# Kernel tuning notes

Measured on AMD Instinct MI355X. Metric: run time of the kernel, lower is better.

Reference implementation:

```python
import jax, jax.numpy as jnp
import numpy as np

B, S, E, H = 4, 8192, 768, 12
Dh = E // H


def setup_inputs() -> dict:
    key = jax.random.key(0)
    ks = jax.random.split(key, 11)
    scale = 1.0 / np.sqrt(E)
    return {
        "query": jax.random.normal(ks[0], (B, S, E), dtype=jnp.float32),
        "key": jax.random.normal(ks[1], (B, S, E), dtype=jnp.float32),
        "value": jax.random.normal(ks[2], (B, S, E), dtype=jnp.float32),
        "Wq": jax.random.normal(ks[3], (E, E), dtype=jnp.float32) * scale,
        "bq": jax.random.normal(ks[4], (E,), dtype=jnp.float32) * scale,
        "Wk": jax.random.normal(ks[5], (E, E), dtype=jnp.float32) * scale,
        "bk": jax.random.normal(ks[6], (E,), dtype=jnp.float32) * scale,
        "Wv": jax.random.normal(ks[7], (E, E), dtype=jnp.float32) * scale,
        "bv": jax.random.normal(ks[8], (E,), dtype=jnp.float32) * scale,
        "Wo": jax.random.normal(ks[9], (E, E), dtype=jnp.float32) * scale,
        "bo": jax.random.normal(ks[10], (E,), dtype=jnp.float32) * scale,
    }


def reference(query, key, value, Wq, bq, Wk, bk, Wv, bv, Wo, bo):
    b, s, e = query.shape
    # torch nn.Linear: x @ W.T + b
    Q = query @ Wq.T + bq  # [B,S,E]
    K = key @ Wk.T + bk
    V = value @ Wv.T + bv
    Q = Q.reshape(b, s, H, Dh)
    K = K.reshape(b, s, H, Dh)
    V = V.reshape(b, s, H, Dh)
    # ReLU feature map on Q and K
    Q = jax.nn.relu(Q)
    K = jax.nn.relu(K)
    # KV aggregation: [B,H,Dh,Dh]
    KV = jnp.einsum('blhd,blhe->bhde', K, V)
    # Query contraction: [B,S,H,Dh]
    QKV = jnp.einsum('blhd,bhde->blhe', Q, KV)
    QKV = QKV.reshape(b, s, e)
    return QKV @ Wo.T + bo
```

## Files before the change

### kernel.cpp

```cpp
#include <hip/hip_runtime.h>
#include <hip/hip_bf16.h>
#include <string.h>


#define H_  12
#define DH  64
#define E_  768
#define S_  8192
#define B_  4

typedef unsigned short u16;
typedef __attribute__((ext_vector_type(4))) float f32x4;
typedef __attribute__((ext_vector_type(4))) u16   u16x4;
typedef __attribute__((ext_vector_type(8))) u16   u16x8;
typedef __attribute__((ext_vector_type(8))) short s16x8;

static __device__ __forceinline__ u16 f2bf(float f) {
    __hip_bfloat16 h = __float2bfloat16(f);
    u16 r; __builtin_memcpy(&r, &h, 2); return r;
}
static __device__ __forceinline__ float bf2f(u16 u) {
    unsigned int i = ((unsigned int)u) << 16;
    float f; __builtin_memcpy(&f, &i, 4); return f;
}

static __device__ __forceinline__ void gload16(const void* g, void* lds) {
    __builtin_amdgcn_global_load_lds(
        (const __attribute__((address_space(1))) unsigned int*)(uintptr_t)g,
        (__attribute__((address_space(3))) unsigned int*)(uintptr_t)lds,
        16, 0, 0);
}

__global__ __launch_bounds__(256) void wconv(const float* __restrict__ in,
                                             u16* __restrict__ out, int n) {
    int i = (blockIdx.x * 256 + threadIdx.x) * 4;
    if (i + 3 < n) {
        f32x4 v = *(const f32x4*)&in[i];
        u16x4 o;
        o[0] = f2bf(v[0]); o[1] = f2bf(v[1]); o[2] = f2bf(v[2]); o[3] = f2bf(v[3]);
        *(u16x4*)&out[i] = o;
    }
}

__global__ __launch_bounds__(256) void xconv(const float* __restrict__ in,
                                             u16* __restrict__ out) {
    long i = ((long)blockIdx.x * 256 + threadIdx.x) * 8;
    f32x4 a = *(const f32x4*)&in[i];
    f32x4 b = *(const f32x4*)&in[i + 4];
    u16x8 o;
    o[0] = f2bf(a[0]); o[1] = f2bf(a[1]); o[2] = f2bf(a[2]); o[3] = f2bf(a[3]);
    o[4] = f2bf(b[0]); o[5] = f2bf(b[1]); o[6] = f2bf(b[2]); o[7] = f2bf(b[3]);
    *(u16x8*)&out[i] = o;
}

template<int RELU, int OUT_F32, int PERB>
__global__ __launch_bounds__(256, 2) void gemm4(const u16* __restrict__ A,
                                                const u16* __restrict__ Bw0,
                                                const float* __restrict__ bias,
                                                void* __restrict__ Cp, int K) {
    __shared__ u16 As[3][4096];
    __shared__ u16 Bs[3][8192];
    const int  t    = threadIdx.x;
    const int  lane = t & 63;
    const int  wave = t >> 6;
    const long m0   = (long)blockIdx.y * 128;
    const long n0   = (long)blockIdx.x * 256;
    const int  wr   = (wave >> 1) * 64;
    const int  wc   = (wave & 1) * 128;
    const int  N    = gridDim.x * 256;
    const u16* Bw   = PERB ? (Bw0 + (long)(blockIdx.y >> 6) * 589824L) : Bw0;

    const u16* srcA[2]; int dstA[2];
    #pragma unroll
    for (int c = 0; c < 2; ++c) {
        int ch   = wave * 2 + c;
        int o    = ch * 1024 + lane * 16;
        int lrow = o >> 7;
        int bir  = (o & 127) ^ ((lrow & 7) << 4);
        int row  = 2 * lrow + (bir >> 6);
        dstA[c]  = ch * 1024;
        srcA[c]  = A + (m0 + row) * (long)K + ((bir & 63) >> 1);
    }
    const u16* srcB[4]; int dstB[4];
    #pragma unroll
    for (int c = 0; c < 4; ++c) {
        int ch   = wave * 4 + c;
        int o    = ch * 1024 + lane * 16;
        int lrow = o >> 7;
        int bir  = (o & 127) ^ ((lrow & 7) << 4);
        int row  = 2 * lrow + (bir >> 6);
        dstB[c]  = ch * 1024;
        srcB[c]  = Bw + (n0 + row) * (long)K + ((bir & 63) >> 1);
    }

    const int kg16 = (lane >> 4) * 16;
    int aoff[4], boff[8];
    #pragma unroll
    for (int mi = 0; mi < 4; ++mi) {
        int m    = wr + mi * 16 + (lane & 15);
        int lrow = m >> 1;
        aoff[mi] = lrow * 128 + ((((m & 1) << 6) | kg16) ^ ((lrow & 7) << 4));
    }
    #pragma unroll
    for (int ni = 0; ni < 8; ++ni) {
        int n    = wc + ni * 16 + (lane & 15);
        int lrow = n >> 1;
        boff[ni] = lrow * 128 + ((((n & 1) << 6) | kg16) ^ ((lrow & 7) << 4));
    }

    f32x4 acc[4][8] = {};

    const int nt = K >> 5;
    #pragma unroll
    for (int c = 0; c < 2; ++c) gload16(srcA[c],      (char*)&As[0][0] + dstA[c]);
    #pragma unroll
    for (int c = 0; c < 4; ++c) gload16(srcB[c],      (char*)&Bs[0][0] + dstB[c]);
    #pragma unroll
    for (int c = 0; c < 2; ++c) gload16(srcA[c] + 32, (char*)&As[1][0] + dstA[c]);
    #pragma unroll
    for (int c = 0; c < 4; ++c) gload16(srcB[c] + 32, (char*)&Bs[1][0] + dstB[c]);

    int sl = 0;
    for (int tt = 0; tt < nt; ++tt) {
        asm volatile("s_waitcnt lgkmcnt(0)" ::: "memory");
        if (tt < nt - 1) asm volatile("s_waitcnt vmcnt(6)" ::: "memory");
        else             asm volatile("s_waitcnt vmcnt(0)" ::: "memory");
        asm volatile("s_barrier" ::: "memory");

        if (tt + 2 < nt) {
            const int  isl = (sl == 0) ? 2 : sl - 1;
            const long k0  = (long)(tt + 2) * 32;
            #pragma unroll
            for (int c = 0; c < 2; ++c) gload16(srcA[c] + k0, (char*)&As[isl][0] + dstA[c]);
            #pragma unroll
            for (int c = 0; c < 4; ++c) gload16(srcB[c] + k0, (char*)&Bs[isl][0] + dstB[c]);
        }

        const char* as = (const char*)&As[sl][0];
        const char* bs = (const char*)&Bs[sl][0];
        s16x8 af[4], bf[8];
        #pragma unroll
        for (int mi = 0; mi < 4; ++mi) af[mi] = *(const s16x8*)(as + aoff[mi]);
        #pragma unroll
        for (int ni = 0; ni < 8; ++ni) bf[ni] = *(const s16x8*)(bs + boff[ni]);

        __builtin_amdgcn_s_setprio(1);
        #pragma unroll
        for (int mi = 0; mi < 4; ++mi)
            #pragma unroll
            for (int ni = 0; ni < 8; ++ni)
                acc[mi][ni] = __builtin_amdgcn_mfma_f32_16x16x32_bf16(af[mi], bf[ni], acc[mi][ni], 0, 0, 0);
        __builtin_amdgcn_s_setprio(0);

        sl = (sl == 2) ? 0 : sl + 1;
    }

    const int cc = lane & 15;
    const int cr = (lane >> 4) * 4;
    float bv[8];
    #pragma unroll
    for (int ni = 0; ni < 8; ++ni) bv[ni] = bias[n0 + wc + ni * 16 + cc];
    #pragma unroll
    for (int mi = 0; mi < 4; ++mi) {
        #pragma unroll
        for (int r = 0; r < 4; ++r) {
            long gm = m0 + wr + mi * 16 + cr + r;
            #pragma unroll
            for (int ni = 0; ni < 8; ++ni) {
                long gn = n0 + wc + ni * 16 + cc;
                float v = acc[mi][ni][r] + bv[ni];
                if (RELU) v = fmaxf(v, 0.0f);
                if (OUT_F32) ((float*)Cp)[gm * N + gn] = v;
                else         ((u16*)Cp)[gm * N + gn]   = f2bf(v);
            }
        }
    }
}

__global__ __launch_bounds__(256) void kv_partial2(const u16* __restrict__ Kb,
                                                   const u16* __restrict__ Vb,
                                                   float* __restrict__ P) {
    __shared__ float sbuf[8192];
    const int bh = blockIdx.x, ch = blockIdx.y;
    const int b = bh / H_, h = bh - b * H_;
    const int t = threadIdx.x, lane = t & 63, wave = t >> 6;
    float* Kf = sbuf + wave * 2048;
    float* Vf = Kf + 1024;
    const long base = ((long)b * S_) * E_ + h * DH;
    const int eB = (lane >> 3) * 8;
    const int dB = (lane & 7) * 8;

    f32x4 acc[8][2] = {};

    const int l0w = ch * 512 + wave * 128;
    for (int ss = 0; ss < 8; ++ss) {
        const int l0 = l0w + ss * 16;
        #pragma unroll
        for (int half = 0; half < 2; ++half) {
            int u  = lane + half * 64;
            int lr = u >> 3, c0 = (u & 7) * 8;
            long g = base + (long)(l0 + lr) * E_ + c0;
            u16x8 kk = *(const u16x8*)&Kb[g];
            u16x8 vv = *(const u16x8*)&Vb[g];
            f32x4 k0, k1, v0, v1;
            #pragma unroll
            for (int j = 0; j < 4; ++j) {
                k0[j] = bf2f(kk[j]); k1[j] = bf2f(kk[j + 4]);
                v0[j] = bf2f(vv[j]); v1[j] = bf2f(vv[j + 4]);
            }
            *(f32x4*)&Kf[lr * 64 + c0]     = k0;
            *(f32x4*)&Kf[lr * 64 + c0 + 4] = k1;
            *(f32x4*)&Vf[lr * 64 + c0]     = v0;
            *(f32x4*)&Vf[lr * 64 + c0 + 4] = v1;
        }
        #pragma unroll
        for (int l = 0; l < 16; ++l) {
            f32x4 e0 = *(const f32x4*)&Vf[l * 64 + eB];
            f32x4 e1 = *(const f32x4*)&Vf[l * 64 + eB + 4];
            f32x4 d0 = *(const f32x4*)&Kf[l * 64 + dB];
            f32x4 d1 = *(const f32x4*)&Kf[l * 64 + dB + 4];
            #pragma unroll
            for (int i = 0; i < 4; ++i) {
                acc[i][0]     += e0[i] * d0;  acc[i][1]     += e0[i] * d1;
                acc[i + 4][0] += e1[i] * d0;  acc[i + 4][1] += e1[i] * d1;
            }
        }
    }

    __syncthreads();
    if (wave >= 2) {
        float* r = sbuf + (wave - 2) * 4096;
        #pragma unroll
        for (int i = 0; i < 8; ++i) {
            *(f32x4*)&r[(eB + i) * 64 + dB]     = acc[i][0];
            *(f32x4*)&r[(eB + i) * 64 + dB + 4] = acc[i][1];
        }
    }
    __syncthreads();
    if (wave < 2) {
        const float* r = sbuf + wave * 4096;
        #pragma unroll
        for (int i = 0; i < 8; ++i) {
            acc[i][0] += *(const f32x4*)&r[(eB + i) * 64 + dB];
            acc[i][1] += *(const f32x4*)&r[(eB + i) * 64 + dB + 4];
        }
    }
    __syncthreads();
    if (wave == 1) {
        #pragma unroll
        for (int i = 0; i < 8; ++i) {
            *(f32x4*)&sbuf[(eB + i) * 64 + dB]     = acc[i][0];
            *(f32x4*)&sbuf[(eB + i) * 64 + dB + 4] = acc[i][1];
        }
    }
    __syncthreads();
    if (wave == 0) {
        float* Pp = &P[((long)(bh * 16 + ch)) * 4096];
        #pragma unroll
        for (int i = 0; i < 8; ++i) {
            f32x4 s0 = acc[i][0] + *(const f32x4*)&sbuf[(eB + i) * 64 + dB];
            f32x4 s1 = acc[i][1] + *(const f32x4*)&sbuf[(eB + i) * 64 + dB + 4];
            *(f32x4*)&Pp[(eB + i) * 64 + dB]     = s0;
            *(f32x4*)&Pp[(eB + i) * 64 + dB + 4] = s1;
        }
    }
}

__global__ __launch_bounds__(256) void kv_reduce2(const float* __restrict__ P,
                                                  u16* __restrict__ KVde) {
    const int bh = blockIdx.x, t = threadIdx.x;
    #pragma unroll
    for (int k = 0; k < 4; ++k) {
        int i = t * 4 + k * 1024;
        f32x4 s = {};
        for (int c = 0; c < 16; ++c) s += *(const f32x4*)&P[((long)(bh * 16 + c)) * 4096 + i];
        const int e = i >> 6, d0 = i & 63;
        #pragma unroll
        for (int j = 0; j < 4; ++j)
            KVde[(long)bh * 4096 + (d0 + j) * 64 + e] = f2bf(s[j]);
    }
}

__global__ __launch_bounds__(256) void w2prep(const u16* __restrict__ Wo_b,
                                              const u16* __restrict__ KVde,
                                              u16* __restrict__ W2t) {
    __shared__ u16 Qs[256 * 64];
    __shared__ u16 Ks[64 * 64];
    const int t = threadIdx.x, lane = t & 63, wave = t >> 6;
    const int h = blockIdx.y, b = blockIdx.z;
    const int n0 = blockIdx.x * 256;

    {
        char* lq = (char*)Qs;
        #pragma unroll
        for (int j = 0; j < 8; ++j) {
            int ob = (wave * 8 + j) * 1024;
            int ol = ob + lane * 16;
            int row = ol >> 7, col = (ol & 127) >> 1;
            gload16(&Wo_b[(long)(n0 + row) * E_ + h * DH + col], lq + ob);
        }
        char* lk = (char*)Ks;
        #pragma unroll
        for (int j = 0; j < 2; ++j) {
            int ob = (wave * 2 + j) * 1024;
            int ol = ob + lane * 16;
            int row = ol >> 7, col = (ol & 127) >> 1;
            gload16(&KVde[((long)(b * H_ + h)) * 4096 + row * 64 + col], lk + ob);
        }
    }
    __syncthreads();

    f32x4 acc[4][4] = {};
    #pragma unroll
    for (int kk = 0; kk < 2; ++kk) {
        s16x8 af[4], bfr[4];
        #pragma unroll
        for (int mi = 0; mi < 4; ++mi)
            af[mi] = *(const s16x8*)&Qs[(wave * 64 + mi * 16 + (lane & 15)) * 64 + kk * 32 + (lane >> 4) * 8];
        #pragma unroll
        for (int ni = 0; ni < 4; ++ni)
            bfr[ni] = *(const s16x8*)&Ks[(ni * 16 + (lane & 15)) * 64 + kk * 32 + (lane >> 4) * 8];
        #pragma unroll
        for (int mi = 0; mi < 4; ++mi)
            #pragma unroll
            for (int ni = 0; ni < 4; ++ni)
                acc[mi][ni] = __builtin_amdgcn_mfma_f32_16x16x32_bf16(af[mi], bfr[ni], acc[mi][ni], 0, 0, 0);
    }

    const int cc = lane & 15, cr = (lane >> 4) * 4;
    u16* Wb = W2t + (long)b * 589824L;
    #pragma unroll
    for (int mi = 0; mi < 4; ++mi) {
        #pragma unroll
        for (int r = 0; r < 4; ++r) {
            long gm = n0 + wave * 64 + mi * 16 + cr + r;
            #pragma unroll
            for (int ni = 0; ni < 4; ++ni)
                Wb[gm * E_ + h * DH + ni * 16 + cc] = f2bf(acc[mi][ni][r]);
        }
    }
}

extern "C" void kernel_launch(void* const* d_in, const int* in_sizes, int n_in,
                              void* d_out, int out_size, void* d_ws, size_t ws_size,
                              hipStream_t stream) {
    const float* q  = (const float*)d_in[0];
    const float* k  = (const float*)d_in[1];
    const float* v  = (const float*)d_in[2];
    const float* Wq = (const float*)d_in[3];
    const float* bq = (const float*)d_in[4];
    const float* Wk = (const float*)d_in[5];
    const float* bk = (const float*)d_in[6];
    const float* Wv = (const float*)d_in[7];
    const float* bv = (const float*)d_in[8];
    const float* Wo = (const float*)d_in[9];
    const float* bo = (const float*)d_in[10];
    float* out = (float*)d_out;

    char* ws = (char*)d_ws;
    u16*   Wq_b = (u16*)(ws);
    u16*   Wk_b = (u16*)(ws + 1179648L);
    u16*   Wv_b = (u16*)(ws + 2359296L);
    u16*   Wo_b = (u16*)(ws + 3538944L);
    u16*   Qb   = (u16*)(ws + 4718592L);
    u16*   Kb   = (u16*)(ws + 55050240L);
    u16*   Vb   = (u16*)(ws + 105381888L);
    float* P    = (float*)(ws + 155713536L);
    u16*   KVde = (u16*)(ws + 168296448L);
    u16*   W2t  = Kb;
    u16*   xb   = (u16*)d_out;

    dim3 blk(256);
    wconv<<<576, blk, 0, stream>>>(Wq, Wq_b, 589824);
    wconv<<<576, blk, 0, stream>>>(Wk, Wk_b, 589824);
    wconv<<<576, blk, 0, stream>>>(Wv, Wv_b, 589824);
    wconv<<<576, blk, 0, stream>>>(Wo, Wo_b, 589824);

    dim3 g1(3, 256);
    xconv<<<12288, blk, 0, stream>>>(q, xb);
    gemm4<1, 0, 0><<<g1, blk, 0, stream>>>(xb, Wq_b, bq, Qb, 768);
    xconv<<<12288, blk, 0, stream>>>(k, xb);
    gemm4<1, 0, 0><<<g1, blk, 0, stream>>>(xb, Wk_b, bk, Kb, 768);
    xconv<<<12288, blk, 0, stream>>>(v, xb);
    gemm4<0, 0, 0><<<g1, blk, 0, stream>>>(xb, Wv_b, bv, Vb, 768);

    kv_partial2<<<dim3(48, 16), blk, 0, stream>>>(Kb, Vb, P);
    kv_reduce2<<<48, blk, 0, stream>>>(P, KVde);
    w2prep<<<dim3(3, 12, 4), blk, 0, stream>>>(Wo_b, KVde, W2t);

    gemm4<0, 1, 1><<<g1, blk, 0, stream>>>(Qb, W2t, bo, out, 768);
}
```

Baseline: 352.3 us.

## Fuse fp32-to-bf16 input conversion into projection GEMM loads with XCD-aware block mapping

Removes the three separate xconv passes by having the GEMM load fp32 activations into registers, convert them to bf16 and write them into swizzled LDS one stage ahead. This avoids a full write and re-read of a bf16 copy of each 100MB input. The launch also becomes a 1D grid remapped so that consecutive M-blocks land on the same XCD, and K is made a compile-time constant with a fully unrolled loop. In exchange, the A tile now goes through registers instead of direct-to-LDS loads, which raises register pressure and puts conversion work in the main loop.

After: 330.4 us, median of 2. 1.07x faster.

```diff
diff --git a/kernel.cpp b/kernel.cpp
--- a/kernel.cpp
+++ b/kernel.cpp
@@ -42,45 +42,28 @@
     }
 }
 
-__global__ __launch_bounds__(256) void xconv(const float* __restrict__ in,
-                                             u16* __restrict__ out) {
-    long i = ((long)blockIdx.x * 256 + threadIdx.x) * 8;
-    f32x4 a = *(const f32x4*)&in[i];
-    f32x4 b = *(const f32x4*)&in[i + 4];
-    u16x8 o;
-    o[0] = f2bf(a[0]); o[1] = f2bf(a[1]); o[2] = f2bf(a[2]); o[3] = f2bf(a[3]);
-    o[4] = f2bf(b[0]); o[5] = f2bf(b[1]); o[6] = f2bf(b[2]); o[7] = f2bf(b[3]);
-    *(u16x8*)&out[i] = o;
-}
-
-template<int RELU, int OUT_F32, int PERB>
-__global__ __launch_bounds__(256, 2) void gemm4(const u16* __restrict__ A,
+template<int AF32, int RELU, int OUT_F32, int PERB>
+__global__ __launch_bounds__(256, 2) void gemm5(const void* __restrict__ Ap,
                                                 const u16* __restrict__ Bw0,
                                                 const float* __restrict__ bias,
-                                                void* __restrict__ Cp, int K) {
+                                                void* __restrict__ Cp) {
+    constexpr int K = 768, NT = 24;
     __shared__ u16 As[3][4096];
     __shared__ u16 Bs[3][8192];
-    const int  t    = threadIdx.x;
-    const int  lane = t & 63;
-    const int  wave = t >> 6;
-    const long m0   = (long)blockIdx.y * 128;
-    const long n0   = (long)blockIdx.x * 256;
-    const int  wr   = (wave >> 1) * 64;
-    const int  wc   = (wave & 1) * 128;
-    const int  N    = gridDim.x * 256;
-    const u16* Bw   = PERB ? (Bw0 + (long)(blockIdx.y >> 6) * 589824L) : Bw0;
-
-    const u16* srcA[2]; int dstA[2];
-    #pragma unroll
-    for (int c = 0; c < 2; ++c) {
-        int ch   = wave * 2 + c;
-        int o    = ch * 1024 + lane * 16;
-        int lrow = o >> 7;
-        int bir  = (o & 127) ^ ((lrow & 7) << 4);
-        int row  = 2 * lrow + (bir >> 6);
-        dstA[c]  = ch * 1024;
-        srcA[c]  = A + (m0 + row) * (long)K + ((bir & 63) >> 1);
-    }
+    const int t = threadIdx.x, lane = t & 63, wave = t >> 6;
+
+    const int phys = blockIdx.x;
+    const int xcd  = phys & 7;
+    const int ii   = phys >> 3;
+    const int i3   = ii / 3;
+    const int mblk = xcd * 32 + i3;
+    const int nblk = ii - i3 * 3;
+    const long m0  = (long)mblk * 128;
+    const long n0  = (long)nblk * 256;
+    const int  wr  = (wave >> 1) * 64;
+    const int  wc  = (wave & 1) * 128;
+    const u16* Bw  = PERB ? (Bw0 + (long)(mblk >> 6) * 589824L) : Bw0;
+
     const u16* srcB[4]; int dstB[4];
     #pragma unroll
     for (int c = 0; c < 4; ++c) {
@@ -92,6 +75,28 @@
         dstB[c]  = ch * 1024;
         srcB[c]  = Bw + (n0 + row) * (long)K + ((bir & 63) >> 1);
     }
+    const u16*   srcA[2]; int dstA[2];
+    const float* aptr = nullptr; int awr0 = 0, awr1 = 0;
+    if constexpr (AF32) {
+        const int ar = t >> 1;
+        const int ac = (t & 1) * 16;
+        aptr = (const float*)Ap + (m0 + ar) * (long)K + ac;
+        const int lrow = ar >> 1;
+        const int kb0  = (t & 1) * 32;
+        awr0 = lrow * 128 + (((((ar & 1) << 6) | (kb0))      ) ^ ((lrow & 7) << 4));
+        awr1 = lrow * 128 + (((((ar & 1) << 6) | (kb0 + 16)) ) ^ ((lrow & 7) << 4));
+    } else {
+        #pragma unroll
+        for (int c = 0; c < 2; ++c) {
+            int ch   = wave * 2 + c;
+            int o    = ch * 1024 + lane * 16;
+            int lrow = o >> 7;
+            int bir  = (o & 127) ^ ((lrow & 7) << 4);
+            int row  = 2 * lrow + (bir >> 6);
+            dstA[c]  = ch * 1024;
+            srcA[c]  = (const u16*)Ap + (m0 + row) * (long)K + ((bir & 63) >> 1);
+        }
+    }
 
     const int kg16 = (lane >> 4) * 16;
     int aoff[4], boff[8];
@@ -109,31 +114,74 @@
     }
 
     f32x4 acc[4][8] = {};
-
-    const int nt = K >> 5;
-    #pragma unroll
-    for (int c = 0; c < 2; ++c) gload16(srcA[c],      (char*)&As[0][0] + dstA[c]);
-    #pragma unroll
-    for (int c = 0; c < 4; ++c) gload16(srcB[c],      (char*)&Bs[0][0] + dstB[c]);
-    #pragma unroll
-    for (int c = 0; c < 2; ++c) gload16(srcA[c] + 32, (char*)&As[1][0] + dstA[c]);
-    #pragma unroll
-    for (int c = 0; c < 4; ++c) gload16(srcB[c] + 32, (char*)&Bs[1][0] + dstB[c]);
-
-    int sl = 0;
-    for (int tt = 0; tt < nt; ++tt) {
+    f32x4 ra[2][4];
+
+    if constexpr (AF32) {
+        #pragma unroll
+        for (int j = 0; j < 4; ++j) ra[0][j] = *(const f32x4*)(aptr + j * 4);
+        #pragma unroll
+        for (int c = 0; c < 4; ++c) gload16(srcB[c], (char*)&Bs[0][0] + dstB[c]);
+        {
+            u16x8 o8;
+            #pragma unroll
+            for (int x = 0; x < 4; ++x) { o8[x] = f2bf(ra[0][0][x]); o8[x + 4] = f2bf(ra[0][1][x]); }
+            *(u16x8*)((char*)&As[0][0] + awr0) = o8;
+            #pragma unroll
+            for (int x = 0; x < 4; ++x) { o8[x] = f2bf(ra[0][2][x]); o8[x + 4] = f2bf(ra[0][3][x]); }
+            *(u16x8*)((char*)&As[0][0] + awr1) = o8;
+        }
+        #pragma unroll
+        for (int j = 0; j < 4; ++j) ra[1][j] = *(const f32x4*)(aptr + 32 + j * 4);
+        #pragma unroll
+        for (int c = 0; c < 4; ++c) gload16(srcB[c] + 32, (char*)&Bs[1][0] + dstB[c]);
+    } else {
+        #pragma unroll
+        for (int c = 0; c < 2; ++c) gload16(srcA[c],      (char*)&As[0][0] + dstA[c]);
+        #pragma unroll
+        for (int c = 0; c < 4; ++c) gload16(srcB[c],      (char*)&Bs[0][0] + dstB[c]);
+        #pragma unroll
+        for (int c = 0; c < 2; ++c) gload16(srcA[c] + 32, (char*)&As[1][0] + dstA[c]);
+        #pragma unroll
+        for (int c = 0; c < 4; ++c) gload16(srcB[c] + 32, (char*)&Bs[1][0] + dstB[c]);
+    }
+
+    #pragma unroll
+    for (int tt = 0; tt < NT; ++tt) {
         asm volatile("s_waitcnt lgkmcnt(0)" ::: "memory");
-        if (tt < nt - 1) asm volatile("s_waitcnt vmcnt(6)" ::: "memory");
-        else             asm volatile("s_waitcnt vmcnt(0)" ::: "memory");
+        if (tt < NT - 1) {
+            if constexpr (AF32) asm volatile("s_waitcnt vmcnt(8)" ::: "memory");
+            else                asm volatile("s_waitcnt vmcnt(6)" ::: "memory");
+        } else {
+            asm volatile("s_waitcnt vmcnt(0)" ::: "memory");
+        }
         asm volatile("s_barrier" ::: "memory");
 
-        if (tt + 2 < nt) {
-            const int  isl = (sl == 0) ? 2 : sl - 1;
-            const long k0  = (long)(tt + 2) * 32;
-            #pragma unroll
-            for (int c = 0; c < 2; ++c) gload16(srcA[c] + k0, (char*)&As[isl][0] + dstA[c]);
+        const int sl = tt % 3;
+        if (tt + 2 < NT) {
+            const int isl = (tt + 2) % 3;
+            const int k0  = (tt + 2) * 32;
+            if constexpr (AF32) {
+                #pragma unroll
+                for (int j = 0; j < 4; ++j) ra[tt & 1][j] = *(const f32x4*)(aptr + k0 + j * 4);
+            } else {
+                #pragma unroll
+                for (int c = 0; c < 2; ++c) gload16(srcA[c] + k0, (char*)&As[isl][0] + dstA[c]);
+            }
             #pragma unroll
             for (int c = 0; c < 4; ++c) gload16(srcB[c] + k0, (char*)&Bs[isl][0] + dstB[c]);
+        }
+        if constexpr (AF32) {
+            if (tt + 1 < NT) {
+                const int wsl = (tt + 1) % 3;
+                const f32x4* rv = ra[(tt + 1) & 1];
+                u16x8 o8;
+                #pragma unroll
+                for (int x = 0; x < 4; ++x) { o8[x] = f2bf(rv[0][x]); o8[x + 4] = f2bf(rv[1][x]); }
+                *(u16x8*)((char*)&As[wsl][0] + awr0) = o8;
+                #pragma unroll
+                for (int x = 0; x < 4; ++x) { o8[x] = f2bf(rv[2][x]); o8[x + 4] = f2bf(rv[3][x]); }
+                *(u16x8*)((char*)&As[wsl][0] + awr1) = o8;
+            }
         }
 
         const char* as = (const char*)&As[sl][0];
@@ -151,8 +199,6 @@
             for (int ni = 0; ni < 8; ++ni)
                 acc[mi][ni] = __builtin_amdgcn_mfma_f32_16x16x32_bf16(af[mi], bf[ni], acc[mi][ni], 0, 0, 0);
         __builtin_amdgcn_s_setprio(0);
-
-        sl = (sl == 2) ? 0 : sl + 1;
     }
 
     const int cc = lane & 15;
@@ -170,8 +216,8 @@
                 long gn = n0 + wc + ni * 16 + cc;
                 float v = acc[mi][ni][r] + bv[ni];
                 if (RELU) v = fmaxf(v, 0.0f);
-                if (OUT_F32) ((float*)Cp)[gm * N + gn] = v;
-                else         ((u16*)Cp)[gm * N + gn]   = f2bf(v);
+                if (OUT_F32) ((float*)Cp)[gm * 768 + gn] = v;
+                else         ((u16*)Cp)[gm * 768 + gn]   = f2bf(v);
             }
         }
     }
@@ -368,7 +414,6 @@
     float* P    = (float*)(ws + 155713536L);
     u16*   KVde = (u16*)(ws + 168296448L);
     u16*   W2t  = Kb;
-    u16*   xb   = (u16*)d_out;
 
     dim3 blk(256);
     wconv<<<576, blk, 0, stream>>>(Wq, Wq_b, 589824);
@@ -376,17 +421,13 @@
     wconv<<<576, blk, 0, stream>>>(Wv, Wv_b, 589824);
     wconv<<<576, blk, 0, stream>>>(Wo, Wo_b, 589824);
 
-    dim3 g1(3, 256);
-    xconv<<<12288, blk, 0, stream>>>(q, xb);
-    gemm4<1, 0, 0><<<g1, blk, 0, stream>>>(xb, Wq_b, bq, Qb, 768);
-    xconv<<<12288, blk, 0, stream>>>(k, xb);
-    gemm4<1, 0, 0><<<g1, blk, 0, stream>>>(xb, Wk_b, bk, Kb, 768);
-    xconv<<<12288, blk, 0, stream>>>(v, xb);
-    gemm4<0, 0, 0><<<g1, blk, 0, stream>>>(xb, Wv_b, bv, Vb, 768);
+    gemm5<1, 1, 0, 0><<<768, blk, 0, stream>>>(q, Wq_b, bq, Qb);
+    gemm5<1, 1, 0, 0><<<768, blk, 0, stream>>>(k, Wk_b, bk, Kb);
+    gemm5<1, 0, 0, 0><<<768, blk, 0, stream>>>(v, Wv_b, bv, Vb);
 
     kv_partial2<<<dim3(48, 16), blk, 0, stream>>>(Kb, Vb, P);
     kv_reduce2<<<48, blk, 0, stream>>>(P, KVde);
     w2prep<<<dim3(3, 12, 4), blk, 0, stream>>>(Wo_b, KVde, W2t);
 
-    gemm4<0, 1, 1><<<g1, blk, 0, stream>>>(Qb, W2t, bo, out, 768);
-}
+    gemm5<0, 0, 1, 1><<<768, blk, 0, stream>>>(Qb, W2t, bo, out);
+}
```
